# Optimization experiments

Hardware: AMD Instinct MI355X
Metric: run time of the kernel (lower is better)

Reference implementation:

```python
import jax, jax.numpy as jnp
import numpy as np

OBS, HID, LAT = 1024, 2048, 256
VOCAB, HQ = 8192, 4
COMMIT = 0.5
N = 16384
LN_EPS = 1e-5


def setup_inputs() -> dict:
    key = jax.random.key(0)
    ks = jax.random.split(key, 7)

    def lin_w(k, fan_in, shape):
        # torch nn.Linear default init: U(-1/sqrt(fan_in), 1/sqrt(fan_in))
        bound = 1.0 / np.sqrt(fan_in)
        return jax.random.uniform(k, shape, jnp.float32, -bound, bound)

    return {
        "x": jax.random.normal(ks[0], (N, OBS), jnp.float32),
        # embeddings initialized uniform(-0.5, 0.5) as in the module
        "codebooks": jax.random.uniform(ks[1], (HQ, VOCAB, LAT), jnp.float32, -0.5, 0.5),
        "enc_w1": lin_w(ks[2], OBS, (OBS, HID)),
        "enc_b1": jnp.zeros((HID,), jnp.float32),
        "ln_g": jnp.ones((HID,), jnp.float32),
        "ln_b": jnp.zeros((HID,), jnp.float32),
        "enc_w2": lin_w(ks[3], HID, (HID, LAT)),
        "enc_b2": jnp.zeros((LAT,), jnp.float32),
        "dec_w1": lin_w(ks[4], LAT, (LAT, HID)),
        "dec_b1": jnp.zeros((HID,), jnp.float32),
        "dec_w2": lin_w(ks[5], HID, (HID, OBS)),
        "dec_b2": jnp.zeros((OBS,), jnp.float32),
    }


def reference(x, codebooks, enc_w1, enc_b1, ln_g, ln_b, enc_w2, enc_b2,
              dec_w1, dec_b1, dec_w2, dec_b2):
    sg = jax.lax.stop_gradient
    # encoder: Linear -> LayerNorm -> ReLU -> Linear
    h = x @ enc_w1 + enc_b1                      # [N, HID]
    mu = h.mean(-1, keepdims=True)
    var = ((h - mu) ** 2).mean(-1, keepdims=True)  # biased var, matches torch LN
    h = (h - mu) * jax.lax.rsqrt(var + LN_EPS) * ln_g + ln_b
    h = jax.nn.relu(h)
    latent = h @ enc_w2 + enc_b2                 # [N, LAT]

    total = jnp.float32(0.0)
    resid = latent
    code_sum = jnp.zeros_like(latent)
    for l in range(HQ):
        E = codebooks[l]                         # [VOCAB, LAT]
        # squared euclidean distances (argmin identical to cdist argmin)
        d2 = ((resid * resid).sum(-1, keepdims=True)
              - 2.0 * (resid @ E.T)
              + (E * E).sum(-1))                 # [N, VOCAB]
        idx = jnp.argmin(d2, axis=-1)            # [N]
        q = E[idx]                               # [N, LAT] gather
        codebook_loss = jnp.mean((q - sg(resid)) ** 2)
        commit_loss = jnp.mean((sg(q) - resid) ** 2)
        total = total + codebook_loss + COMMIT * commit_loss
        code_sum = code_sum + q
        resid = resid - q

    # straight-through estimator
    quant = latent + sg(code_sum - latent)
    # decoder: Linear -> ReLU -> Linear
    dh = jax.nn.relu(quant @ dec_w1 + dec_b1)
    recon = dh @ dec_w2 + dec_b2                 # [N, OBS]
    total = total + 0.5 * jnp.mean((recon - x) ** 2)
    return total
```

## Files before the change

kernel.cpp:

```cpp
#include <hip/hip_runtime.h>

#define N_ROWS 16384
#define OBS    1024
#define HID    2048
#define LAT    256
#define VOCAB  8192
#define HQ     4
#define LN_EPS 1e-5f

typedef unsigned short u16;
typedef unsigned long long u64;
typedef __bf16 bf16x8 __attribute__((ext_vector_type(8)));
typedef float  f32x4  __attribute__((ext_vector_type(4)));

static __device__ __forceinline__ unsigned int float_to_ordered(float f) {
    unsigned int u = __float_as_uint(f);
    return (u & 0x80000000u) ? ~u : (u | 0x80000000u);
}
static __device__ __forceinline__ u16 f2bf(float f) {
    unsigned int u = __float_as_uint(f);
    unsigned int r = u + 0x7FFFu + ((u >> 16) & 1u);
    return (u16)(r >> 16);
}
static __device__ __forceinline__ float bf2f(u16 u) {
    return __uint_as_float((unsigned int)u << 16);
}

#define GL2LDS(gp, lp) __builtin_amdgcn_global_load_lds( \
    (const __attribute__((address_space(1))) void*)(gp), \
    (__attribute__((address_space(3))) void*)(lp), 16, 0, 0)

template<int EPI>
__global__ __launch_bounds__(256, 4) void mfma_gemm_k(
    const u16* __restrict__ Abf, const u16* __restrict__ Bbf,
    const float* __restrict__ bias,
    u16* __restrict__ Cbf,
    const float* __restrict__ X, double* __restrict__ lacc,
    int K, int Nd)
{
    __shared__ u16 As[128 * 64];
    __shared__ u16 Bs[128 * 64];

    const int tid  = threadIdx.x;
    const int wv   = tid >> 6, lane = tid & 63;
    const int wm   = wv & 1,   wn   = wv >> 1;
    const int m_   = lane & 15, g   = lane >> 4;
    const int m0   = blockIdx.x * 128;
    const int n0   = blockIdx.y * 128;

    f32x4 acc[4][4];
#pragma unroll
    for (int i = 0; i < 4; ++i)
#pragma unroll
        for (int j = 0; j < 4; ++j)
            acc[i][j] = f32x4{0.f, 0.f, 0.f, 0.f};

    const u16* Ablk = Abf + (size_t)m0 * K;
    const u16* Bblk = Bbf + (size_t)n0 * K;

    for (int k0 = 0; k0 < K; k0 += 64) {
#pragma unroll
        for (int c = 0; c < 4; ++c) {
            const int ci = (wv * 4 + c) * 64 + lane;
            const int r  = ci >> 3;
            const int cc = ci & 7;
            const int kc = (cc ^ (r & 7)) << 3;
            GL2LDS(Ablk + (size_t)r * K + k0 + kc, As + (wv * 4 + c) * 512);
            GL2LDS(Bblk + (size_t)r * K + k0 + kc, Bs + (wv * 4 + c) * 512);
        }
        __syncthreads();
#pragma unroll
        for (int ks = 0; ks < 2; ++ks) {
            const int ccw = ks * 4 + g;
            const int sw  = (ccw ^ (m_ & 7)) << 3;
            bf16x8 af[4], bfr[4];
#pragma unroll
            for (int t = 0; t < 4; ++t) {
                af[t]  = *(const bf16x8*)&As[(wm * 64 + t * 16 + m_) * 64 + sw];
                bfr[t] = *(const bf16x8*)&Bs[(wn * 64 + t * 16 + m_) * 64 + sw];
            }
#pragma unroll
            for (int mi = 0; mi < 4; ++mi)
#pragma unroll
                for (int ni = 0; ni < 4; ++ni)
                    acc[mi][ni] = __builtin_amdgcn_mfma_f32_16x16x32_bf16(
                        af[mi], bfr[ni], acc[mi][ni], 0, 0, 0);
        }
        __syncthreads();
    }

    float bs[4];
#pragma unroll
    for (int ni = 0; ni < 4; ++ni) bs[ni] = bias[n0 + wn * 64 + ni * 16 + m_];

    if constexpr (EPI == 3) {
        float lsum = 0.f;
#pragma unroll
        for (int mi = 0; mi < 4; ++mi)
#pragma unroll
            for (int j = 0; j < 4; ++j) {
                const int row = m0 + wm * 64 + mi * 16 + g * 4 + j;
#pragma unroll
                for (int ni = 0; ni < 4; ++ni) {
                    const int col = n0 + wn * 64 + ni * 16 + m_;
                    float r = acc[mi][ni][j] + bs[ni] - X[(size_t)row * Nd + col];
                    lsum = fmaf(r, r, lsum);
                }
            }
#pragma unroll
        for (int off = 32; off >= 1; off >>= 1) lsum += __shfl_xor(lsum, off);
        __shared__ float red[4];
        if (lane == 0) red[wv] = lsum;
        __syncthreads();
        if (tid == 0)
            atomicAdd(lacc, (double)(red[0] + red[1] + red[2] + red[3]));
    } else {
#pragma unroll
        for (int mi = 0; mi < 4; ++mi)
#pragma unroll
            for (int j = 0; j < 4; ++j) {
                const int row = m0 + wm * 64 + mi * 16 + g * 4 + j;
#pragma unroll
                for (int ni = 0; ni < 4; ++ni) {
                    const int col = n0 + wn * 64 + ni * 16 + m_;
                    float v = acc[mi][ni][j] + bs[ni];
                    if constexpr (EPI == 1) v = fmaxf(v, 0.f);
                    Cbf[(size_t)row * Nd + col] = f2bf(v);
                }
            }
    }
}

__global__ __launch_bounds__(256, 4) void gemm2_k(
    const u16* __restrict__ Abf, const u16* __restrict__ Bbf,
    const float* __restrict__ bias,
    float* __restrict__ lat, float* __restrict__ resid, u16* __restrict__ rbf)
{
    __shared__ u16 As[64 * 64];
    __shared__ u16 Bs[64 * 64];

    const int tid = threadIdx.x;
    const int wv  = tid >> 6, lane = tid & 63;
    const int wm  = wv & 1,   wn   = wv >> 1;
    const int m_  = lane & 15, g   = lane >> 4;
    const int m0  = blockIdx.x * 64;
    const int n0  = blockIdx.y * 64;

    f32x4 acc[2][2];
#pragma unroll
    for (int i = 0; i < 2; ++i)
#pragma unroll
        for (int j = 0; j < 2; ++j)
            acc[i][j] = f32x4{0.f, 0.f, 0.f, 0.f};

    const u16* Ablk = Abf + (size_t)m0 * HID;
    const u16* Bblk = Bbf + (size_t)n0 * HID;

    for (int k0 = 0; k0 < HID; k0 += 64) {
#pragma unroll
        for (int c = 0; c < 2; ++c) {
            const int ci = (wv * 2 + c) * 64 + lane;
            const int r  = ci >> 3;
            const int cc = ci & 7;
            const int kc = (cc ^ (r & 7)) << 3;
            GL2LDS(Ablk + (size_t)r * HID + k0 + kc, As + (wv * 2 + c) * 512);
            GL2LDS(Bblk + (size_t)r * HID + k0 + kc, Bs + (wv * 2 + c) * 512);
        }
        __syncthreads();
#pragma unroll
        for (int ks = 0; ks < 2; ++ks) {
            const int ccw = ks * 4 + g;
            const int sw  = (ccw ^ (m_ & 7)) << 3;
            bf16x8 af[2], bfr[2];
#pragma unroll
            for (int t = 0; t < 2; ++t) {
                af[t]  = *(const bf16x8*)&As[(wm * 32 + t * 16 + m_) * 64 + sw];
                bfr[t] = *(const bf16x8*)&Bs[(wn * 32 + t * 16 + m_) * 64 + sw];
            }
#pragma unroll
            for (int mi = 0; mi < 2; ++mi)
#pragma unroll
                for (int ni = 0; ni < 2; ++ni)
                    acc[mi][ni] = __builtin_amdgcn_mfma_f32_16x16x32_bf16(
                        af[mi], bfr[ni], acc[mi][ni], 0, 0, 0);
        }
        __syncthreads();
    }

#pragma unroll
    for (int mi = 0; mi < 2; ++mi)
#pragma unroll
        for (int j = 0; j < 4; ++j) {
            const int row = m0 + wm * 32 + mi * 16 + g * 4 + j;
#pragma unroll
            for (int ni = 0; ni < 2; ++ni) {
                const int col = n0 + wn * 32 + ni * 16 + m_;
                float v = acc[mi][ni][j] + bias[col];
                lat  [(size_t)row * LAT + col] = v;
                resid[(size_t)row * LAT + col] = v;
                rbf  [(size_t)row * LAT + col] = f2bf(v);
            }
        }
}

__global__ __launch_bounds__(256) void tpose4_k(
    const float* __restrict__ W0, u16* __restrict__ T0,
    const float* __restrict__ W1, u16* __restrict__ T1,
    const float* __restrict__ W2, u16* __restrict__ T2,
    const float* __restrict__ W3, u16* __restrict__ T3)
{
    __shared__ u16 t[32][33];
    const int bid = blockIdx.x;
    const float* W; u16* T; int K, N, r;
    if (bid < 2048)      { W = W0; T = T0; K = OBS; N = HID; r = bid; }
    else if (bid < 2560) { W = W1; T = T1; K = HID; N = LAT; r = bid - 2048; }
    else if (bid < 3072) { W = W2; T = T2; K = LAT; N = HID; r = bid - 2560; }
    else                 { W = W3; T = T3; K = HID; N = OBS; r = bid - 3072; }
    const int nb = N >> 5;
    const int n0 = (r % nb) * 32, k0 = (r / nb) * 32;
    const int lx = threadIdx.x & 31, ly = threadIdx.x >> 5;
#pragma unroll
    for (int i = 0; i < 4; ++i)
        t[ly + 8 * i][lx] = f2bf(W[(size_t)(k0 + ly + 8 * i) * N + n0 + lx]);
    __syncthreads();
#pragma unroll
    for (int i = 0; i < 4; ++i)
        T[(size_t)(n0 + ly + 8 * i) * K + k0 + lx] = t[lx][ly + 8 * i];
}

__device__ __forceinline__ float block_reduce_bcast(float v, float* scratch) {
#pragma unroll
    for (int off = 32; off >= 1; off >>= 1) v += __shfl_xor(v, off);
    const int tid = threadIdx.x;
    __syncthreads();
    if ((tid & 63) == 0) scratch[tid >> 6] = v;
    __syncthreads();
    return scratch[0] + scratch[1] + scratch[2] + scratch[3];
}

__global__ __launch_bounds__(256) void ln_relu_bf_k(
    u16* __restrict__ h, const float* __restrict__ g, const float* __restrict__ b)
{
    __shared__ float scratch[4];
    const int tid = threadIdx.x;
    u16* hp = h + (size_t)blockIdx.x * HID + tid * 8;

    ushort4 r0 = *(const ushort4*)hp;
    ushort4 r1 = *(const ushort4*)(hp + 4);
    float v[8] = {bf2f(r0.x), bf2f(r0.y), bf2f(r0.z), bf2f(r0.w),
                  bf2f(r1.x), bf2f(r1.y), bf2f(r1.z), bf2f(r1.w)};

    float s = 0.f;
#pragma unroll
    for (int e = 0; e < 8; ++e) s += v[e];
    const float mu = block_reduce_bcast(s, scratch) * (1.f / HID);

    float vs = 0.f;
#pragma unroll
    for (int e = 0; e < 8; ++e) { float d = v[e] - mu; vs = fmaf(d, d, vs); }
    const float var = block_reduce_bcast(vs, scratch) * (1.f / HID);
    const float rs = rsqrtf(var + LN_EPS);

    ushort4 o0, o1;
#pragma unroll
    for (int e = 0; e < 8; ++e) {
        const int col = tid * 8 + e;
        float w = (v[e] - mu) * rs * g[col] + b[col];
        w = fmaxf(w, 0.f);
        u16 bb = f2bf(w);
        if (e < 4) ((u16*)&o0)[e] = bb; else ((u16*)&o1)[e - 4] = bb;
    }
    *(ushort4*)hp = o0;
    *(ushort4*)(hp + 4) = o1;
}

__global__ __launch_bounds__(256) void enorm_k(
    const float* __restrict__ cb, float* __restrict__ enorm,
    u16* __restrict__ cbb, u64* __restrict__ keys, double* __restrict__ accs)
{
    if (blockIdx.x < 64) keys[blockIdx.x * 256 + threadIdx.x] = ~0ull;
    if (blockIdx.x == 64 && threadIdx.x < 2) accs[threadIdx.x] = 0.0;
    const int row  = blockIdx.x * 4 + (threadIdx.x >> 6);
    const int lane = threadIdx.x & 63;
    const size_t off = (size_t)row * LAT + lane * 4;
    float4 v = *(const float4*)(cb + off);
    ushort4 o;
    o.x = f2bf(-2.f * v.x); o.y = f2bf(-2.f * v.y);
    o.z = f2bf(-2.f * v.z); o.w = f2bf(-2.f * v.w);
    *(ushort4*)(cbb + off) = o;
    float s = v.x * v.x + v.y * v.y + v.z * v.z + v.w * v.w;
#pragma unroll
    for (int off2 = 32; off2 >= 1; off2 >>= 1) s += __shfl_xor(s, off2);
    if (lane == 0) enorm[row] = s;
}

__global__ __launch_bounds__(256) void f2bf_k(
    const float* __restrict__ in, u16* __restrict__ out)
{
    size_t i = ((size_t)blockIdx.x * 256 + threadIdx.x) * 4;
    float4 v = *(const float4*)(in + i);
    ushort4 o;
    o.x = f2bf(v.x); o.y = f2bf(v.y); o.z = f2bf(v.z); o.w = f2bf(v.w);
    *(ushort4*)(out + i) = o;
}

#define DNT 16

__global__ __launch_bounds__(256, 2) void dist_mfma_k(
    const u16* __restrict__ Abf, const u16* __restrict__ Bneg2,
    const float* __restrict__ enorm, u64* __restrict__ keys)
{
    __shared__ u16 Bs[2][64 * 256];
    __shared__ u64 shk[128][2];

    const int tid  = threadIdx.x;
    const int wv   = tid >> 6, lane = tid & 63;
    const int wm   = wv & 1,   wn   = wv >> 1;
    const int m_   = lane & 15, g   = lane >> 4;
    const int m0   = blockIdx.x * 128;
    const int c0   = blockIdx.y * (64 * DNT);

    bf16x8 af[4][8];
    {
        const u16* Ablk = Abf + (size_t)m0 * LAT;
#pragma unroll
        for (int mi = 0; mi < 4; ++mi) {
            const u16* rp = Ablk + (size_t)(wm * 64 + mi * 16 + m_) * LAT + g * 8;
#pragma unroll
            for (int kk = 0; kk < 8; ++kk)
                af[mi][kk] = *(const bf16x8*)(rp + kk * 32);
        }
    }

    const u16* Bbase = Bneg2 + (size_t)c0 * LAT;

    float bestf[4][4];
    int   besti[4][4];
#pragma unroll
    for (int mi = 0; mi < 4; ++mi)
#pragma unroll
        for (int j4 = 0; j4 < 4; ++j4) {
            bestf[mi][j4] = __int_as_float(0x7f800000);
            besti[mi][j4] = 0;
        }

    auto stageB = [&](int j, int buf) {
#pragma unroll
        for (int t = 0; t < 4; ++t)
#pragma unroll
            for (int c = 0; c < 2; ++c) {
                const int idx = (wv * 2 + c) * 64 + lane;
                const int r   = idx >> 3;
                const int cc  = idx & 7;
                const int kc  = (cc ^ (r & 7)) << 3;
                GL2LDS(Bbase + (size_t)(j * 64 + r) * LAT + t * 64 + kc,
                       &Bs[buf][t * 4096 + (wv * 2 + c) * 512]);
            }
    };

    stageB(0, 0);

    const int ecol = wn * 32 + m_;
    float enA = enorm[c0 + ecol];
    float enB = enorm[c0 + ecol + 16];

    __syncthreads();

    for (int j = 0; j < DNT; ++j) {
        const int cur = j & 1;
        if (j + 1 < DNT) stageB(j + 1, cur ^ 1);

        float enA_n = 0.f, enB_n = 0.f;
        if (j + 1 < DNT) {
            enA_n = enorm[c0 + (j + 1) * 64 + ecol];
            enB_n = enorm[c0 + (j + 1) * 64 + ecol + 16];
        }

        const int bc = c0 + j * 64 + ecol;
        f32x4 acc[4][2];
#pragma unroll
        for (int mi = 0; mi < 4; ++mi) {
            acc[mi][0] = f32x4{enA, enA, enA, enA};
            acc[mi][1] = f32x4{enB, enB, enB, enB};
        }

        const u16* bsc = &Bs[cur][0];
#pragma unroll
        for (int kc_ = 0; kc_ < 4; ++kc_)
#pragma unroll
            for (int ks = 0; ks < 2; ++ks) {
                const int ccw = ks * 4 + g;
                const int sw  = (ccw ^ (m_ & 7)) << 3;
                bf16x8 b0 = *(const bf16x8*)
                    &bsc[kc_ * 4096 + (wn * 32 + m_) * 64 + sw];
                bf16x8 b1 = *(const bf16x8*)
                    &bsc[kc_ * 4096 + (wn * 32 + 16 + m_) * 64 + sw];
                const int kk = kc_ * 2 + ks;
#pragma unroll
                for (int mi = 0; mi < 4; ++mi) {
                    acc[mi][0] = __builtin_amdgcn_mfma_f32_16x16x32_bf16(
                        af[mi][kk], b0, acc[mi][0], 0, 0, 0);
                    acc[mi][1] = __builtin_amdgcn_mfma_f32_16x16x32_bf16(
                        af[mi][kk], b1, acc[mi][1], 0, 0, 0);
                }
            }

#pragma unroll
        for (int mi = 0; mi < 4; ++mi)
#pragma unroll
            for (int j4 = 0; j4 < 4; ++j4) {
                const float s0 = acc[mi][0][j4];
                const float s1 = acc[mi][1][j4];
                if (s0 < bestf[mi][j4]) { bestf[mi][j4] = s0; besti[mi][j4] = bc; }
                if (s1 < bestf[mi][j4]) { bestf[mi][j4] = s1; besti[mi][j4] = bc + 16; }
            }

        enA = enA_n; enB = enB_n;
        __syncthreads();
    }

#pragma unroll
    for (int mi = 0; mi < 4; ++mi)
#pragma unroll
        for (int j4 = 0; j4 < 4; ++j4) {
            u64 b = ((u64)float_to_ordered(bestf[mi][j4]) << 32)
                  | (unsigned)besti[mi][j4];
#pragma unroll
            for (int mask = 1; mask <= 8; mask <<= 1) {
                u64 o = __shfl_xor(b, mask);
                b = o < b ? o : b;
            }
            if (m_ == 0) shk[wm * 64 + mi * 16 + g * 4 + j4][wn] = b;
        }
    __syncthreads();
    if (tid < 128) {
        u64 a = shk[tid][0], b = shk[tid][1];
        atomicMin(&keys[m0 + tid], a < b ? a : b);
    }
}

template<bool LAST>
__global__ __launch_bounds__(256) void vq_update_k(
    float* __restrict__ resid, u16* __restrict__ aux,
    const float* __restrict__ latent,
    const float* __restrict__ E,
    u64* __restrict__ keys, double* __restrict__ acc)
{
    __shared__ float red[4];
    const int tid = threadIdx.x;
    const int base = blockIdx.x * 16;
    float lsum = 0.f;
    for (int r = 0; r < 16; ++r) {
        const int row = base + r;
        const int idx = (int)(keys[row] & 0xFFFFFFFFull);
        const float q = E[(size_t)idx * LAT + tid];
        float v = resid[(size_t)row * LAT + tid] - q;
        if constexpr (LAST) {
            aux[(size_t)row * LAT + tid] =
                f2bf(latent[(size_t)row * LAT + tid] - v);
        } else {
            resid[(size_t)row * LAT + tid] = v;
            aux[(size_t)row * LAT + tid] = f2bf(v);
        }
        lsum = fmaf(v, v, lsum);
    }
    if (!LAST && tid < 16) keys[base + tid] = ~0ull;
#pragma unroll
    for (int off = 32; off >= 1; off >>= 1) lsum += __shfl_xor(lsum, off);
    if ((tid & 63) == 0) red[tid >> 6] = lsum;
    __syncthreads();
    if (tid == 0) atomicAdd(acc, (double)(red[0] + red[1] + red[2] + red[3]));
}

__global__ void finalize_k(const double* __restrict__ acc, float* __restrict__ out) {
    double total = 1.5 * acc[0] / (double)((size_t)N_ROWS * LAT)
                 + 0.5 * acc[1] / (double)((size_t)N_ROWS * OBS);
    out[0] = (float)total;
}

extern "C" void kernel_launch(void* const* d_in, const int* in_sizes, int n_in,
                              void* d_out, int out_size, void* d_ws, size_t ws_size,
                              hipStream_t stream)
{
    const float* x      = (const float*)d_in[0];
    const float* cb     = (const float*)d_in[1];
    const float* enc_w1 = (const float*)d_in[2];
    const float* enc_b1 = (const float*)d_in[3];
    const float* ln_g   = (const float*)d_in[4];
    const float* ln_b   = (const float*)d_in[5];
    const float* enc_w2 = (const float*)d_in[6];
    const float* enc_b2 = (const float*)d_in[7];
    const float* dec_w1 = (const float*)d_in[8];
    const float* dec_b1 = (const float*)d_in[9];
    const float* dec_w2 = (const float*)d_in[10];
    const float* dec_b2 = (const float*)d_in[11];

    char* ws = (char*)d_ws;
    const size_t MB = 1ull << 20;
    u16* hbuf = (u16*)ws;
    u16* cbb  = (u16*)(ws + 64 * MB);
    u16* rbf  = (u16*)(ws + 80 * MB);
    u16* qbf  = (u16*)(ws + 88 * MB);
    u16* xbf  = (u16*)(ws + 96 * MB);
    float* latent = (float*)(ws + 96 * MB);
    float* resid  = (float*)(ws + 112 * MB);
    u16* w1T  = (u16*)(ws + 128 * MB);
    u16* w2T  = (u16*)(ws + 132 * MB);
    u16* wd1T = (u16*)(ws + 133 * MB);
    u16* wd2T = (u16*)(ws + 134 * MB);
    float* enorm = (float*)(ws + 138 * MB);
    u64*   keys  = (u64*)(ws + 138 * MB + 131072);
    double* accs = (double*)(ws + 138 * MB + 262144);

    enorm_k<<<HQ * VOCAB / 4, 256, 0, stream>>>(cb, enorm, cbb, keys, accs);

    tpose4_k<<<5120, 256, 0, stream>>>(enc_w1, w1T, enc_w2, w2T,
                                       dec_w1, wd1T, dec_w2, wd2T);
    f2bf_k<<<(int)((size_t)N_ROWS * OBS / 1024), 256, 0, stream>>>(x, xbf);

    mfma_gemm_k<0><<<dim3(N_ROWS / 128, HID / 128), 256, 0, stream>>>(
        xbf, w1T, enc_b1, hbuf, nullptr, nullptr, OBS, HID);
    ln_relu_bf_k<<<N_ROWS, 256, 0, stream>>>(hbuf, ln_g, ln_b);
    gemm2_k<<<dim3(N_ROWS / 64, LAT / 64), 256, 0, stream>>>(
        hbuf, w2T, enc_b2, latent, resid, rbf);

    for (int l = 0; l < HQ; ++l) {
        dist_mfma_k<<<dim3(N_ROWS / 128, VOCAB / (64 * DNT)), 256, 0, stream>>>(
            rbf, cbb + (size_t)l * VOCAB * LAT, enorm + (size_t)l * VOCAB, keys);
        if (l < HQ - 1)
            vq_update_k<false><<<N_ROWS / 16, 256, 0, stream>>>(
                resid, rbf, nullptr, cb + (size_t)l * VOCAB * LAT, keys, accs);
        else
            vq_update_k<true><<<N_ROWS / 16, 256, 0, stream>>>(
                resid, qbf, latent, cb + (size_t)l * VOCAB * LAT, keys, accs);
    }

    mfma_gemm_k<1><<<dim3(N_ROWS / 128, HID / 128), 256, 0, stream>>>(
        qbf, wd1T, dec_b1, hbuf, nullptr, nullptr, LAT, HID);
    mfma_gemm_k<3><<<dim3(N_ROWS / 128, OBS / 128), 256, 0, stream>>>(
        hbuf, wd2T, dec_b2, nullptr, x, accs + 1, HID, OBS);

    finalize_k<<<1, 1, 0, stream>>>(accs, (float*)d_out);
}
```

Baseline: 804.8 us.

## Triple-buffer codebook tiles with 32-column steps and LDS-staged norms in distance kernel

Reworks the distance/argmin kernel to stage 32 codebook rows per step into a three-deep LDS ring buffer, prefetching two tiles ahead with explicit vmcnt waits and a raw barrier. The codebook norms are now loaded once per block into LDS instead of read from global memory each step, and the MFMA section is bracketed with raised wave priority. The intent is to hide global-to-LDS latency and cut barrier stalls. The trade-off is half as much MFMA work per barrier, since each wave now computes one 16-column slice per step instead of two. Each block covers the same 1024 columns, so the grid size is unchanged.

```diff
diff --git a/kernel.cpp b/kernel.cpp
--- a/kernel.cpp
+++ b/kernel.cpp
@@ -304,13 +304,14 @@
     *(ushort4*)(out + i) = o;
 }
 
-#define DNT 16
+#define DNT 32
 
 __global__ __launch_bounds__(256, 2) void dist_mfma_k(
     const u16* __restrict__ Abf, const u16* __restrict__ Bneg2,
     const float* __restrict__ enorm, u64* __restrict__ keys)
 {
-    __shared__ u16 Bs[2][64 * 256];
+    __shared__ u16 Bs[3][32 * 256];
+    __shared__ float en_lds[32 * DNT];
     __shared__ u64 shk[128][2];
 
     const int tid  = threadIdx.x;
@@ -318,7 +319,7 @@
     const int wm   = wv & 1,   wn   = wv >> 1;
     const int m_   = lane & 15, g   = lane >> 4;
     const int m0   = blockIdx.x * 128;
-    const int c0   = blockIdx.y * (64 * DNT);
+    const int c0   = blockIdx.y * (32 * DNT);
 
     bf16x8 af[4][8];
     {
@@ -346,77 +347,74 @@
 
     auto stageB = [&](int j, int buf) {
 #pragma unroll
+        for (int t = 0; t < 4; ++t) {
+            const int idx = wv * 64 + lane;
+            const int r   = idx >> 3;
+            const int cc  = idx & 7;
+            const int kc  = (cc ^ (r & 7)) << 3;
+            GL2LDS(Bbase + (size_t)(j * 32 + r) * LAT + t * 64 + kc,
+                   &Bs[buf][t * 2048 + wv * 512]);
+        }
+    };
+
+    GL2LDS(enorm + c0 + wv * 256 + lane * 4, en_lds + wv * 256);
+    stageB(0, 0);
+    stageB(1, 1);
+    asm volatile("s_waitcnt vmcnt(4)" ::: "memory");
+    __builtin_amdgcn_s_barrier();
+    asm volatile("" ::: "memory");
+
+    const int ecol = wn * 16 + m_;
+
+    int cur = 0, nx2 = 2;
+#pragma unroll 1
+    for (int j = 0; j < DNT; ++j) {
+        if (j + 2 < DNT) {
+            stageB(j + 2, nx2);
+            asm volatile("s_waitcnt vmcnt(4)" ::: "memory");
+        } else {
+            asm volatile("s_waitcnt vmcnt(0)" ::: "memory");
+        }
+
+        const int bc = c0 + j * 32 + ecol;
+        const float en = en_lds[j * 32 + ecol];
+        f32x4 acc[4];
+#pragma unroll
+        for (int mi = 0; mi < 4; ++mi)
+            acc[mi] = f32x4{en, en, en, en};
+
+        const u16* bsc = &Bs[cur][0];
+        __builtin_amdgcn_s_setprio(1);
+#pragma unroll
         for (int t = 0; t < 4; ++t)
-#pragma unroll
-            for (int c = 0; c < 2; ++c) {
-                const int idx = (wv * 2 + c) * 64 + lane;
-                const int r   = idx >> 3;
-                const int cc  = idx & 7;
-                const int kc  = (cc ^ (r & 7)) << 3;
-                GL2LDS(Bbase + (size_t)(j * 64 + r) * LAT + t * 64 + kc,
-                       &Bs[buf][t * 4096 + (wv * 2 + c) * 512]);
-            }
-    };
-
-    stageB(0, 0);
-
-    const int ecol = wn * 32 + m_;
-    float enA = enorm[c0 + ecol];
-    float enB = enorm[c0 + ecol + 16];
-
-    __syncthreads();
-
-    for (int j = 0; j < DNT; ++j) {
-        const int cur = j & 1;
-        if (j + 1 < DNT) stageB(j + 1, cur ^ 1);
-
-        float enA_n = 0.f, enB_n = 0.f;
-        if (j + 1 < DNT) {
-            enA_n = enorm[c0 + (j + 1) * 64 + ecol];
-            enB_n = enorm[c0 + (j + 1) * 64 + ecol + 16];
-        }
-
-        const int bc = c0 + j * 64 + ecol;
-        f32x4 acc[4][2];
-#pragma unroll
-        for (int mi = 0; mi < 4; ++mi) {
-            acc[mi][0] = f32x4{enA, enA, enA, enA};
-            acc[mi][1] = f32x4{enB, enB, enB, enB};
-        }
-
-        const u16* bsc = &Bs[cur][0];
-#pragma unroll
-        for (int kc_ = 0; kc_ < 4; ++kc_)
 #pragma unroll
             for (int ks = 0; ks < 2; ++ks) {
                 const int ccw = ks * 4 + g;
                 const int sw  = (ccw ^ (m_ & 7)) << 3;
                 bf16x8 b0 = *(const bf16x8*)
-                    &bsc[kc_ * 4096 + (wn * 32 + m_) * 64 + sw];
-                bf16x8 b1 = *(const bf16x8*)
-                    &bsc[kc_ * 4096 + (wn * 32 + 16 + m_) * 64 + sw];
-                const int kk = kc_ * 2 + ks;
-#pragma unroll
-                for (int mi = 0; mi < 4; ++mi) {
-                    acc[mi][0] = __builtin_amdgcn_mfma_f32_16x16x32_bf16(
-                        af[mi][kk], b0, acc[mi][0], 0, 0, 0);
-                    acc[mi][1] = __builtin_amdgcn_mfma_f32_16x16x32_bf16(
-                        af[mi][kk], b1, acc[mi][1], 0, 0, 0);
-                }
-            }
+                    &bsc[t * 2048 + (wn * 16 + m_) * 64 + sw];
+                const int kk = t * 2 + ks;
+#pragma unroll
+                for (int mi = 0; mi < 4; ++mi)
+                    acc[mi] = __builtin_amdgcn_mfma_f32_16x16x32_bf16(
+                        af[mi][kk], b0, acc[mi], 0, 0, 0);
+            }
+        __builtin_amdgcn_s_setprio(0);
 
 #pragma unroll
         for (int mi = 0; mi < 4; ++mi)
 #pragma unroll
             for (int j4 = 0; j4 < 4; ++j4) {
-                const float s0 = acc[mi][0][j4];
-                const float s1 = acc[mi][1][j4];
+                const float s0 = acc[mi][j4];
                 if (s0 < bestf[mi][j4]) { bestf[mi][j4] = s0; besti[mi][j4] = bc; }
-                if (s1 < bestf[mi][j4]) { bestf[mi][j4] = s1; besti[mi][j4] = bc + 16; }
-            }
-
-        enA = enA_n; enB = enB_n;
-        __syncthreads();
+            }
+
+        asm volatile("" ::: "memory");
+        __builtin_amdgcn_s_barrier();
+        asm volatile("" ::: "memory");
+
+        cur = (cur == 2) ? 0 : cur + 1;
+        nx2 = (nx2 == 2) ? 0 : nx2 + 1;
     }
 
 #pragma unroll
@@ -525,7 +523,7 @@
         hbuf, w2T, enc_b2, latent, resid, rbf);
 
     for (int l = 0; l < HQ; ++l) {
-        dist_mfma_k<<<dim3(N_ROWS / 128, VOCAB / (64 * DNT)), 256, 0, stream>>>(
+        dist_mfma_k<<<dim3(N_ROWS / 128, VOCAB / (32 * DNT)), 256, 0, stream>>>(
             rbf, cbb + (size_t)l * VOCAB * LAT, enorm + (size_t)l * VOCAB, keys);
         if (l < HQ - 1)
             vq_update_k<false><<<N_ROWS / 16, 256, 0, stream>>>(
```

New measurement: 833.8 us. 1.04x slower.

## Load codebook tiles directly into registers instead of staging through LDS

Applied to the files above, without the earlier changes.

The distance kernel no longer stages codebook tiles into shared memory with async global-to-LDS copies and block barriers. Each wave now loads its own B fragments from global memory into registers, with a two-buffer prefetch across K chunks and tiles. This removes the per-tile __syncthreads and frees LDS, which may allow higher occupancy. In exchange, the two waves sharing columns load the same data twice, global reads are less coalesced, and register pressure rises.

```diff
diff --git a/kernel.cpp b/kernel.cpp
--- a/kernel.cpp
+++ b/kernel.cpp
@@ -310,7 +310,6 @@
     const u16* __restrict__ Abf, const u16* __restrict__ Bneg2,
     const float* __restrict__ enorm, u64* __restrict__ keys)
 {
-    __shared__ u16 Bs[2][64 * 256];
     __shared__ u64 shk[128][2];
 
     const int tid  = threadIdx.x;
@@ -332,8 +331,6 @@
         }
     }
 
-    const u16* Bbase = Bneg2 + (size_t)c0 * LAT;
-
     float bestf[4][4];
     int   besti[4][4];
 #pragma unroll
@@ -344,32 +341,27 @@
             besti[mi][j4] = 0;
         }
 
-    auto stageB = [&](int j, int buf) {
-#pragma unroll
-        for (int t = 0; t < 4; ++t)
-#pragma unroll
-            for (int c = 0; c < 2; ++c) {
-                const int idx = (wv * 2 + c) * 64 + lane;
-                const int r   = idx >> 3;
-                const int cc  = idx & 7;
-                const int kc  = (cc ^ (r & 7)) << 3;
-                GL2LDS(Bbase + (size_t)(j * 64 + r) * LAT + t * 64 + kc,
-                       &Bs[buf][t * 4096 + (wv * 2 + c) * 512]);
-            }
+    const u16* Bbase = Bneg2 + (size_t)c0 * LAT;
+    const int  colA  = wn * 32 + m_;
+    const int  kofs  = g * 8;
+
+    auto loadChunk = [&](int j, int kc, bf16x8* d) {
+        const u16* p = Bbase + (size_t)(j * 64 + colA) * LAT + kc * 64 + kofs;
+        d[0] = *(const bf16x8*)(p);
+        d[1] = *(const bf16x8*)(p + (size_t)16 * LAT);
+        d[2] = *(const bf16x8*)(p + 32);
+        d[3] = *(const bf16x8*)(p + 32 + (size_t)16 * LAT);
     };
 
-    stageB(0, 0);
+    bf16x8 bufA[4], bufB[4];
+    loadChunk(0, 0, bufA);
 
     const int ecol = wn * 32 + m_;
     float enA = enorm[c0 + ecol];
     float enB = enorm[c0 + ecol + 16];
 
-    __syncthreads();
-
+#pragma unroll 1
     for (int j = 0; j < DNT; ++j) {
-        const int cur = j & 1;
-        if (j + 1 < DNT) stageB(j + 1, cur ^ 1);
-
         float enA_n = 0.f, enB_n = 0.f;
         if (j + 1 < DNT) {
             enA_n = enorm[c0 + (j + 1) * 64 + ecol];
@@ -384,18 +376,20 @@
             acc[mi][1] = f32x4{enB, enB, enB, enB};
         }
 
-        const u16* bsc = &Bs[cur][0];
-#pragma unroll
-        for (int kc_ = 0; kc_ < 4; ++kc_)
+#pragma unroll
+        for (int kc = 0; kc < 4; ++kc) {
+            bf16x8* cur = (kc & 1) ? bufB : bufA;
+            bf16x8* nxt = (kc & 1) ? bufA : bufB;
+            if (kc < 3) {
+                loadChunk(j, kc + 1, nxt);
+            } else if (j + 1 < DNT) {
+                loadChunk(j + 1, 0, nxt);
+            }
 #pragma unroll
             for (int ks = 0; ks < 2; ++ks) {
-                const int ccw = ks * 4 + g;
-                const int sw  = (ccw ^ (m_ & 7)) << 3;
-                bf16x8 b0 = *(const bf16x8*)
-                    &bsc[kc_ * 4096 + (wn * 32 + m_) * 64 + sw];
-                bf16x8 b1 = *(const bf16x8*)
-                    &bsc[kc_ * 4096 + (wn * 32 + 16 + m_) * 64 + sw];
-                const int kk = kc_ * 2 + ks;
+                const int kk = kc * 2 + ks;
+                const bf16x8 b0 = cur[2 * ks];
+                const bf16x8 b1 = cur[2 * ks + 1];
 #pragma unroll
                 for (int mi = 0; mi < 4; ++mi) {
                     acc[mi][0] = __builtin_amdgcn_mfma_f32_16x16x32_bf16(
@@ -404,6 +398,7 @@
                         af[mi][kk], b1, acc[mi][1], 0, 0, 0);
                 }
             }
+        }
 
 #pragma unroll
         for (int mi = 0; mi < 4; ++mi)
@@ -416,7 +411,6 @@
             }
 
         enA = enA_n; enB = enB_n;
-        __syncthreads();
     }
 
 #pragma unroll
```

New measurement: 977.9 us. 1.21x slower.
